# Kernel optimization log

Measured on AMD Instinct MI355X. Metric: run time of the kernel, lower is better.

## Reference

```python
import jax, jax.numpy as jnp
import numpy as np

D_MODEL = 1024
NUM_HEADS = 16
HEAD_DIM = D_MODEL // NUM_HEADS


def setup_inputs() -> dict:
    key = jax.random.key(0)
    ks = jax.random.split(key, 10)
    s = 1.0 / np.sqrt(D_MODEL)
    x = jax.random.normal(ks[0], (2, 2048, D_MODEL), dtype=jnp.float32)
    mask = jax.random.randint(ks[1], (1, 1, 2048, 2048), 0, 2, dtype=jnp.int32)
    Wq = jax.random.uniform(ks[2], (D_MODEL, D_MODEL), jnp.float32, -s, s)
    bq = jnp.zeros((D_MODEL,), jnp.float32)
    Wk = jax.random.uniform(ks[3], (D_MODEL, D_MODEL), jnp.float32, -s, s)
    bk = jnp.zeros((D_MODEL,), jnp.float32)
    Wv = jax.random.uniform(ks[4], (D_MODEL, D_MODEL), jnp.float32, -s, s)
    bv = jnp.zeros((D_MODEL,), jnp.float32)
    Wo = jax.random.uniform(ks[5], (D_MODEL, D_MODEL), jnp.float32, -s, s)
    bo = jnp.zeros((D_MODEL,), jnp.float32)
    return {"x": x, "mask": mask, "Wq": Wq, "bq": bq, "Wk": Wk, "bk": bk,
            "Wv": Wv, "bv": bv, "Wo": Wo, "bo": bo}


def reference(x, mask, Wq, bq, Wk, bk, Wv, bv, Wo, bo):
    B, S, D = x.shape
    # Q/K/V projections, split into heads: [B, H, S, Dh]
    q = (x @ Wq + bq).reshape(B, S, NUM_HEADS, HEAD_DIM).transpose(0, 2, 1, 3)
    k = (x @ Wk + bk).reshape(B, S, NUM_HEADS, HEAD_DIM).transpose(0, 2, 1, 3)
    v = (x @ Wv + bv).reshape(B, S, NUM_HEADS, HEAD_DIM).transpose(0, 2, 1, 3)
    # scores: [B, H, S, S]
    scores = jnp.einsum('bhqd,bhkd->bhqk', q, k) / np.sqrt(HEAD_DIM).astype(np.float32)
    scores = jnp.where(mask == 0, jnp.float32(-1e9), scores)
    weights = jax.nn.softmax(scores, axis=-1)
    # dropout is identity in eval / p=0
    context = jnp.einsum('bhqk,bhkd->bhqd', weights, v)
    context = context.transpose(0, 2, 1, 3).reshape(B, S, D)
    return context @ Wo + bo
```

## Files before the change

kernel.cpp:

```cpp
#include <hip/hip_runtime.h>
#include <stdint.h>

typedef unsigned short u16;
typedef unsigned int u32;
typedef u16 u16x4 __attribute__((ext_vector_type(4)));
typedef u16 u16x8 __attribute__((ext_vector_type(8)));
typedef u32 u32x4 __attribute__((ext_vector_type(4)));
typedef __bf16 bf16x8 __attribute__((ext_vector_type(8)));
typedef float f32x4 __attribute__((ext_vector_type(4)));

#define GLL16(g, l) __builtin_amdgcn_global_load_lds( \
    (const __attribute__((address_space(1))) void*)(g), \
    (__attribute__((address_space(3))) void*)(l), 16, 0, 0)

#define QSCALE 0.18033688011112042f

__device__ __forceinline__ u16 f2bf(float f) {
  u32 u = __builtin_bit_cast(u32, f);
  u += 0x7fffu + ((u >> 16) & 1u);
  return (u16)(u >> 16);
}
__device__ __forceinline__ bf16x8 asbf(u16x8 v) { return __builtin_bit_cast(bf16x8, v); }

__global__ void k_cvt_x(const float* __restrict__ x, u16* __restrict__ o) {
  int i = blockIdx.x * 256 + threadIdx.x;
  f32x4 v = ((const f32x4*)x)[i];
  u16x4 r = { f2bf(v[0]), f2bf(v[1]), f2bf(v[2]), f2bf(v[3]) };
  ((u16x4*)o)[i] = r;
}

__global__ void k_cvt_wT(const float* __restrict__ w, u16* __restrict__ wt, float scale) {
  __shared__ float t[32][33];
  int k0 = blockIdx.x << 5, n0 = blockIdx.y << 5;
  int lx = threadIdx.x & 31, ly = threadIdx.x >> 5;
  #pragma unroll
  for (int i = 0; i < 4; ++i)
    t[ly + 8*i][lx] = w[(size_t)(k0 + ly + 8*i) * 1024 + n0 + lx];
  __syncthreads();
  #pragma unroll
  for (int i = 0; i < 4; ++i)
    wt[(size_t)(n0 + ly + 8*i) * 1024 + k0 + lx] = f2bf(t[lx][ly + 8*i] * scale);
}

__global__ void k_bias(const float* __restrict__ bq, const float* __restrict__ bk,
                       const float* __restrict__ bv, float* __restrict__ o) {
  int i = blockIdx.x * 256 + threadIdx.x;
  float v;
  if (i < 1024) v = bq[i] * QSCALE;
  else if (i < 2048) v = bk[i - 1024];
  else v = bv[i - 2048];
  o[i] = v;
}

__global__ void k_maskbits(const int* __restrict__ mask, u32* __restrict__ bits) {
  int w = blockIdx.x * 256 + threadIdx.x;
  const int* src = mask + (size_t)w * 32;
  u32 b = 0;
  #pragma unroll
  for (int i = 0; i < 32; ++i) b |= (src[i] != 0 ? 1u : 0u) << i;
  bits[w] = b;
}

__global__ __launch_bounds__(256) void k_vT(const u16* __restrict__ vws, u16* __restrict__ vtws) {
  __shared__ u16 t[64][72];
  const int bh = blockIdx.x;
  const int st = blockIdx.y;
  const int tid = threadIdx.x;
  {
    const int s = tid >> 2, c4 = (tid & 3) << 4;
    const u16* src = vws + ((size_t)bh * 2048 + st * 64 + s) * 64 + c4;
    *(u16x8*)&t[s][c4] = *(const u16x8*)src;
    *(u16x8*)&t[s][c4 + 8] = *(const u16x8*)(src + 8);
  }
  __syncthreads();
  {
    const int d = tid >> 2, s0 = (tid & 3) << 4;
    u16 tmp[16];
    #pragma unroll
    for (int j = 0; j < 16; ++j) tmp[j] = t[s0 + j][d];
    u16* dst = vtws + ((size_t)bh * 64 + d) * 2048 + st * 64 + s0;
    *(u16x8*)dst = *(u16x8*)&tmp[0];
    *(u16x8*)(dst + 8) = *(u16x8*)&tmp[8];
  }
}

template<int EPI>
__global__ __launch_bounds__(256)
void k_gemm(const u16* __restrict__ A, const u16* __restrict__ Bt,
            const float* __restrict__ bias, float* __restrict__ outF,
            u16* __restrict__ qws, u16* __restrict__ kws, u16* __restrict__ vws)
{
  __shared__ u16 As[128 * 32];
  __shared__ u16 Bs[128 * 32];
  const int tid = threadIdx.x;
  const int lane = tid & 63;
  const int wv = tid >> 6;
  const int g = lane >> 4, cc = lane & 15;
  const int wr = wv >> 1, wc = wv & 1;
  const int bm = blockIdx.y, bn = blockIdx.x;

  f32x4 acc[4][4] = {};

  for (int k0 = 0; k0 < 1024; k0 += 32) {
    __syncthreads();
    #pragma unroll
    for (int call = 0; call < 2; ++call) {
      int idx = call * 256 + tid;
      int row = idx >> 2;
      int sw = ((idx & 3) << 4) ^ ((row & 3) << 4);
      GLL16((const char*)(A + (size_t)(bm * 128 + row) * 1024 + k0) + sw,
            (char*)As + (call * 256 + wv * 64) * 16);
      GLL16((const char*)(Bt + (size_t)(bn * 128 + row) * 1024 + k0) + sw,
            (char*)Bs + (call * 256 + wv * 64) * 16);
    }
    __syncthreads();

    u16x8 a[4], b[4];
    #pragma unroll
    for (int m = 0; m < 4; ++m) {
      int row = wr * 64 + m * 16 + cc;
      a[m] = *(const u16x8*)((const char*)As + row * 64 + ((g * 16) ^ ((row & 3) << 4)));
    }
    #pragma unroll
    for (int n = 0; n < 4; ++n) {
      int row = wc * 64 + n * 16 + cc;
      b[n] = *(const u16x8*)((const char*)Bs + row * 64 + ((g * 16) ^ ((row & 3) << 4)));
    }
    #pragma unroll
    for (int m = 0; m < 4; ++m)
      #pragma unroll
      for (int n = 0; n < 4; ++n)
        acc[m][n] = __builtin_amdgcn_mfma_f32_16x16x32_bf16(asbf(a[m]), asbf(b[n]), acc[m][n], 0, 0, 0);
  }

  if constexpr (EPI == 1) {
    #pragma unroll
    for (int m = 0; m < 4; ++m) {
      int Mrow0 = bm * 128 + wr * 64 + m * 16 + g * 4;
      #pragma unroll
      for (int n = 0; n < 4; ++n) {
        int Ncol = bn * 128 + wc * 64 + n * 16 + cc;
        float bvv = bias[Ncol];
        #pragma unroll
        for (int r = 0; r < 4; ++r)
          outF[(size_t)(Mrow0 + r) * 1024 + Ncol] = acc[m][n][r] + bvv;
      }
    }
  } else {
    #pragma unroll
    for (int n = 0; n < 4; ++n) {
      int Ncol = bn * 128 + wc * 64 + n * 16 + cc;
      float bvv = bias[Ncol];
      int which = Ncol >> 10;
      int h = (Ncol >> 6) & 15;
      int d = Ncol & 63;
      u16* bp = which == 0 ? qws : (which == 1 ? kws : vws);
      #pragma unroll
      for (int m = 0; m < 4; ++m) {
        int Mrow0 = bm * 128 + wr * 64 + m * 16 + g * 4;
        int bb = Mrow0 >> 11;
        int s0 = Mrow0 & 2047;
        u16* dst = bp + ((size_t)(bb * 16 + h) * 2048 + s0) * 64 + d;
        #pragma unroll
        for (int r = 0; r < 4; ++r) dst[(size_t)r * 64] = f2bf(acc[m][n][r] + bvv);
      }
    }
  }
}

__global__ __launch_bounds__(256, 4)
void k_attn(const u16* __restrict__ qws, const u16* __restrict__ kws,
            const u16* __restrict__ vtws, const u32* __restrict__ mbits,
            u16* __restrict__ ctx)
{
  __shared__ u16 Kt[2][64 * 64];
  __shared__ u16 Vt[2][64 * 64];

  const int tid = threadIdx.x;
  const int lane = tid & 63;
  const int wv = tid >> 6;
  const int g = lane >> 4;
  const int cc = lane & 15;
  const int blk = blockIdx.x;
  const int qc = blk & 31;
  const int bh = blk >> 5;
  const int b = bh >> 4, h = bh & 15;
  const size_t base = (size_t)bh * (2048 * 64);
  const int qrow = qc * 64 + wv * 16;

  u16x8 qf0, qf1;
  {
    const u16* qp = qws + base + (size_t)(qrow + cc) * 64 + g * 8;
    qf0 = *(const u16x8*)qp;
    qf1 = *(const u16x8*)(qp + 32);
  }
  const u32* mq = mbits + (size_t)(qrow + cc) * 64;

  f32x4 oacc[4] = {};
  float lrun = 0.f;

  auto STAGE = [&](int bufi, int kb) {
    #pragma unroll
    for (int call = 0; call < 2; ++call) {
      int idx = call * 256 + tid;
      int row = idx >> 3;
      int sw = ((idx & 7) << 4) ^ ((row & 7) << 4);
      int krow = (row & 32) + (((row >> 2) & 3) << 3) + (((row >> 4) & 1) << 2) + (row & 3);
      GLL16((const char*)(kws + base + (size_t)(kb + krow) * 64) + sw,
            (char*)&Kt[bufi][0] + (call * 256 + wv * 64) * 16);
      GLL16((const char*)(vtws + base + (size_t)row * 2048 + kb) + sw,
            (char*)&Vt[bufi][0] + (call * 256 + wv * 64) * 16);
    }
  };

  STAGE(0, 0);
  __syncthreads();

  int cur = 0;
  for (int kb = 0; kb < 2048; kb += 64) {
    if (kb + 64 < 2048) STAGE(cur ^ 1, kb + 64);

    uint2 mw2 = *(const uint2*)(mq + (kb >> 5));
    u32 m0 = mw2.x >> (g * 8);
    u32 m1 = mw2.y >> (g * 8);

    f32x4 sc[4];
    #pragma unroll
    for (int t = 0; t < 4; ++t) {
      int row = t * 16 + cc;
      int swz = (row & 7) << 4;
      const char* kr = (const char*)&Kt[cur][0] + row * 128;
      u16x8 kf0 = *(const u16x8*)(kr + ((g * 16) ^ swz));
      u16x8 kf1 = *(const u16x8*)(kr + ((g * 16 + 64) ^ swz));
      f32x4 s = {};
      s = __builtin_amdgcn_mfma_f32_16x16x32_bf16(asbf(kf0), asbf(qf0), s, 0, 0, 0);
      s = __builtin_amdgcn_mfma_f32_16x16x32_bf16(asbf(kf1), asbf(qf1), s, 0, 0, 0);
      sc[t] = s;
    }

    float rs = 0.f;
    #pragma unroll
    for (int t = 0; t < 4; ++t) {
      u32 msel = (t >> 1) ? m1 : m0;
      #pragma unroll
      for (int r = 0; r < 4; ++r) {
        float pv = exp2f(sc[t][r]);
        u32 bit = (msel >> (4 * (t & 1) + r)) & 1u;
        pv = bit ? pv : 0.0f;
        sc[t][r] = pv;
        rs += pv;
      }
    }
    u32 pk[8];
    #pragma unroll
    for (int t = 0; t < 4; ++t) {
      u32 w0, w1;
      asm("v_cvt_pk_bf16_f32 %0, %1, %2" : "=v"(w0) : "v"(sc[t][0]), "v"(sc[t][1]));
      asm("v_cvt_pk_bf16_f32 %0, %1, %2" : "=v"(w1) : "v"(sc[t][2]), "v"(sc[t][3]));
      pk[2 * t] = w0;
      pk[2 * t + 1] = w1;
    }
    rs += __shfl_xor(rs, 16);
    rs += __shfl_xor(rs, 32);
    lrun += rs;

    #pragma unroll
    for (int ch = 0; ch < 2; ++ch) {
      u32x4 pw = { pk[4 * ch], pk[4 * ch + 1], pk[4 * ch + 2], pk[4 * ch + 3] };
      u16x8 pa = __builtin_bit_cast(u16x8, pw);
      #pragma unroll
      for (int f = 0; f < 4; ++f) {
        int row = f * 16 + cc;
        int swz = (row & 7) << 4;
        u16x8 vf = *(const u16x8*)((const char*)&Vt[cur][0] + row * 128 + ((g * 16 + ch * 64) ^ swz));
        oacc[f] = __builtin_amdgcn_mfma_f32_16x16x32_bf16(asbf(pa), asbf(vf), oacc[f], 0, 0, 0);
      }
    }

    __syncthreads();
    cur ^= 1;
  }

  float inv = 1.0f / lrun;
  float i_o[4];
  #pragma unroll
  for (int r = 0; r < 4; ++r) i_o[r] = __shfl(inv, 4 * g + r);
  #pragma unroll
  for (int f = 0; f < 4; ++f)
    #pragma unroll
    for (int r = 0; r < 4; ++r) {
      int q = qrow + 4 * g + r;
      ctx[((size_t)(b * 2048 + q)) * 1024 + h * 64 + f * 16 + cc] = f2bf(oacc[f][r] * i_o[r]);
    }
}

extern "C" void kernel_launch(void* const* d_in, const int* in_sizes, int n_in,
                              void* d_out, int out_size, void* d_ws, size_t ws_size,
                              hipStream_t stream) {
  (void)in_sizes; (void)n_in; (void)out_size; (void)ws_size;
  const float* x   = (const float*)d_in[0];
  const int*  mask = (const int*)d_in[1];
  const float* Wq  = (const float*)d_in[2];
  const float* bq  = (const float*)d_in[3];
  const float* Wk  = (const float*)d_in[4];
  const float* bk  = (const float*)d_in[5];
  const float* Wv  = (const float*)d_in[6];
  const float* bv  = (const float*)d_in[7];
  const float* Wo  = (const float*)d_in[8];
  const float* bo  = (const float*)d_in[9];

  char* p = (char*)d_ws;
  size_t off = 0;
  auto carve = [&](size_t n) { char* r = p + off; off = (off + n + 255) & ~(size_t)255; return r; };
  u16*  xb    = (u16*)carve((size_t)4096 * 1024 * 2);
  u16*  wqkvt = (u16*)carve((size_t)3072 * 1024 * 2);
  u16*  wot   = (u16*)carve((size_t)1024 * 1024 * 2);
  float* bqkv = (float*)carve(3072 * 4);
  u32*  mbits = (u32*)carve((size_t)2048 * 64 * 4);
  u16*  qws   = (u16*)carve((size_t)32 * 2048 * 64 * 2);
  u16*  kws   = (u16*)carve((size_t)32 * 2048 * 64 * 2);
  u16*  vws   = (u16*)carve((size_t)32 * 2048 * 64 * 2);
  u16*  vtws  = (u16*)carve((size_t)32 * 2048 * 64 * 2);
  u16*  ctx   = (u16*)carve((size_t)4096 * 1024 * 2);

  k_cvt_x<<<dim3(4096), dim3(256), 0, stream>>>(x, xb);
  k_cvt_wT<<<dim3(32, 32), dim3(256), 0, stream>>>(Wq, wqkvt, QSCALE);
  k_cvt_wT<<<dim3(32, 32), dim3(256), 0, stream>>>(Wk, wqkvt + 1024 * 1024, 1.0f);
  k_cvt_wT<<<dim3(32, 32), dim3(256), 0, stream>>>(Wv, wqkvt + 2 * 1024 * 1024, 1.0f);
  k_cvt_wT<<<dim3(32, 32), dim3(256), 0, stream>>>(Wo, wot, 1.0f);
  k_bias<<<dim3(12), dim3(256), 0, stream>>>(bq, bk, bv, bqkv);
  k_maskbits<<<dim3(512), dim3(256), 0, stream>>>(mask, mbits);

  k_gemm<0><<<dim3(24, 32), dim3(256), 0, stream>>>(xb, wqkvt, bqkv, nullptr, qws, kws, vws);
  k_vT<<<dim3(32, 32), dim3(256), 0, stream>>>(vws, vtws);
  k_attn<<<dim3(1024), dim3(256), 0, stream>>>(qws, kws, vtws, mbits, ctx);
  k_gemm<1><<<dim3(8, 32), dim3(256), 0, stream>>>(ctx, wot, bo, (float*)d_out, nullptr, nullptr, nullptr);
}
```

Measured before the change: 244.3 us.

## Process two 16-row query tiles per wave in attention to reuse K/V LDS loads

Each attention wave now handles 32 query rows (two 16-row tiles) instead of 16, so each block covers 128 queries and the grid halves to 512 blocks. The K and V fragments read from shared memory and the staged K/V tiles are reused across both query tiles, halving LDS reads and global K/V staging per query. The masking select is also replaced with a sign-extended bitfield AND. In exchange, register pressure roughly doubles for accumulators and there are fewer blocks, so fewer waves are available to fill the 256 CUs and hide latency.

```diff
diff --git a/kernel.cpp b/kernel.cpp
--- a/kernel.cpp
+++ b/kernel.cpp
@@ -182,22 +182,26 @@
   const int g = lane >> 4;
   const int cc = lane & 15;
   const int blk = blockIdx.x;
-  const int qc = blk & 31;
-  const int bh = blk >> 5;
+  const int qc = blk & 15;
+  const int bh = blk >> 4;
   const int b = bh >> 4, h = bh & 15;
   const size_t base = (size_t)bh * (2048 * 64);
-  const int qrow = qc * 64 + wv * 16;
-
-  u16x8 qf0, qf1;
+  const int qrow = qc * 128 + wv * 32;
+
+  u16x8 qfA0, qfA1, qfB0, qfB1;
   {
-    const u16* qp = qws + base + (size_t)(qrow + cc) * 64 + g * 8;
-    qf0 = *(const u16x8*)qp;
-    qf1 = *(const u16x8*)(qp + 32);
-  }
-  const u32* mq = mbits + (size_t)(qrow + cc) * 64;
-
-  f32x4 oacc[4] = {};
-  float lrun = 0.f;
+    const u16* qpA = qws + base + (size_t)(qrow + cc) * 64 + g * 8;
+    qfA0 = *(const u16x8*)qpA;
+    qfA1 = *(const u16x8*)(qpA + 32);
+    const u16* qpB = qpA + 16 * 64;
+    qfB0 = *(const u16x8*)qpB;
+    qfB1 = *(const u16x8*)(qpB + 32);
+  }
+  const u32* mqA = mbits + (size_t)(qrow + cc) * 64;
+  const u32* mqB = mqA + 16 * 64;
+
+  f32x4 oaccA[4] = {}, oaccB[4] = {};
+  float lrunA = 0.f, lrunB = 0.f;
 
   auto STAGE = [&](int bufi, int kb) {
     #pragma unroll
@@ -220,11 +224,12 @@
   for (int kb = 0; kb < 2048; kb += 64) {
     if (kb + 64 < 2048) STAGE(cur ^ 1, kb + 64);
 
-    uint2 mw2 = *(const uint2*)(mq + (kb >> 5));
-    u32 m0 = mw2.x >> (g * 8);
-    u32 m1 = mw2.y >> (g * 8);
-
-    f32x4 sc[4];
+    uint2 mwA = *(const uint2*)(mqA + (kb >> 5));
+    uint2 mwB = *(const uint2*)(mqB + (kb >> 5));
+    u32 mA0 = mwA.x >> (g * 8), mA1 = mwA.y >> (g * 8);
+    u32 mB0 = mwB.x >> (g * 8), mB1 = mwB.y >> (g * 8);
+
+    f32x4 scA[4], scB[4];
     #pragma unroll
     for (int t = 0; t < 4; ++t) {
       int row = t * 16 + cc;
@@ -232,48 +237,61 @@
       const char* kr = (const char*)&Kt[cur][0] + row * 128;
       u16x8 kf0 = *(const u16x8*)(kr + ((g * 16) ^ swz));
       u16x8 kf1 = *(const u16x8*)(kr + ((g * 16 + 64) ^ swz));
-      f32x4 s = {};
-      s = __builtin_amdgcn_mfma_f32_16x16x32_bf16(asbf(kf0), asbf(qf0), s, 0, 0, 0);
-      s = __builtin_amdgcn_mfma_f32_16x16x32_bf16(asbf(kf1), asbf(qf1), s, 0, 0, 0);
-      sc[t] = s;
-    }
-
-    float rs = 0.f;
+      f32x4 sA = {}, sB = {};
+      sA = __builtin_amdgcn_mfma_f32_16x16x32_bf16(asbf(kf0), asbf(qfA0), sA, 0, 0, 0);
+      sA = __builtin_amdgcn_mfma_f32_16x16x32_bf16(asbf(kf1), asbf(qfA1), sA, 0, 0, 0);
+      sB = __builtin_amdgcn_mfma_f32_16x16x32_bf16(asbf(kf0), asbf(qfB0), sB, 0, 0, 0);
+      sB = __builtin_amdgcn_mfma_f32_16x16x32_bf16(asbf(kf1), asbf(qfB1), sB, 0, 0, 0);
+      scA[t] = sA;
+      scB[t] = sB;
+    }
+
+    u32 pkA[8], pkB[8];
+    float rsA = 0.f, rsB = 0.f;
     #pragma unroll
     for (int t = 0; t < 4; ++t) {
-      u32 msel = (t >> 1) ? m1 : m0;
+      u32 mselA = (t >> 1) ? mA1 : mA0;
+      u32 mselB = (t >> 1) ? mB1 : mB0;
       #pragma unroll
       for (int r = 0; r < 4; ++r) {
-        float pv = exp2f(sc[t][r]);
-        u32 bit = (msel >> (4 * (t & 1) + r)) & 1u;
-        pv = bit ? pv : 0.0f;
-        sc[t][r] = pv;
-        rs += pv;
+        int sh = 4 * (t & 1) + r;
+        float pA = exp2f(scA[t][r]);
+        float pB = exp2f(scB[t][r]);
+        u32 mmA = (u32)__builtin_amdgcn_sbfe((int)mselA, sh, 1);
+        u32 mmB = (u32)__builtin_amdgcn_sbfe((int)mselB, sh, 1);
+        pA = __builtin_bit_cast(float, __builtin_bit_cast(u32, pA) & mmA);
+        pB = __builtin_bit_cast(float, __builtin_bit_cast(u32, pB) & mmB);
+        scA[t][r] = pA; rsA += pA;
+        scB[t][r] = pB; rsB += pB;
       }
-    }
-    u32 pk[8];
-    #pragma unroll
-    for (int t = 0; t < 4; ++t) {
       u32 w0, w1;
-      asm("v_cvt_pk_bf16_f32 %0, %1, %2" : "=v"(w0) : "v"(sc[t][0]), "v"(sc[t][1]));
-      asm("v_cvt_pk_bf16_f32 %0, %1, %2" : "=v"(w1) : "v"(sc[t][2]), "v"(sc[t][3]));
-      pk[2 * t] = w0;
-      pk[2 * t + 1] = w1;
-    }
-    rs += __shfl_xor(rs, 16);
-    rs += __shfl_xor(rs, 32);
-    lrun += rs;
+      asm("v_cvt_pk_bf16_f32 %0, %1, %2" : "=v"(w0) : "v"(scA[t][0]), "v"(scA[t][1]));
+      asm("v_cvt_pk_bf16_f32 %0, %1, %2" : "=v"(w1) : "v"(scA[t][2]), "v"(scA[t][3]));
+      pkA[2 * t] = w0; pkA[2 * t + 1] = w1;
+      asm("v_cvt_pk_bf16_f32 %0, %1, %2" : "=v"(w0) : "v"(scB[t][0]), "v"(scB[t][1]));
+      asm("v_cvt_pk_bf16_f32 %0, %1, %2" : "=v"(w1) : "v"(scB[t][2]), "v"(scB[t][3]));
+      pkB[2 * t] = w0; pkB[2 * t + 1] = w1;
+    }
+    rsA += __shfl_xor(rsA, 16);
+    rsA += __shfl_xor(rsA, 32);
+    rsB += __shfl_xor(rsB, 16);
+    rsB += __shfl_xor(rsB, 32);
+    lrunA += rsA;
+    lrunB += rsB;
 
     #pragma unroll
     for (int ch = 0; ch < 2; ++ch) {
-      u32x4 pw = { pk[4 * ch], pk[4 * ch + 1], pk[4 * ch + 2], pk[4 * ch + 3] };
-      u16x8 pa = __builtin_bit_cast(u16x8, pw);
+      u32x4 pwA = { pkA[4 * ch], pkA[4 * ch + 1], pkA[4 * ch + 2], pkA[4 * ch + 3] };
+      u32x4 pwB = { pkB[4 * ch], pkB[4 * ch + 1], pkB[4 * ch + 2], pkB[4 * ch + 3] };
+      u16x8 paA = __builtin_bit_cast(u16x8, pwA);
+      u16x8 paB = __builtin_bit_cast(u16x8, pwB);
       #pragma unroll
       for (int f = 0; f < 4; ++f) {
         int row = f * 16 + cc;
         int swz = (row & 7) << 4;
         u16x8 vf = *(const u16x8*)((const char*)&Vt[cur][0] + row * 128 + ((g * 16 + ch * 64) ^ swz));
-        oacc[f] = __builtin_amdgcn_mfma_f32_16x16x32_bf16(asbf(pa), asbf(vf), oacc[f], 0, 0, 0);
+        oaccA[f] = __builtin_amdgcn_mfma_f32_16x16x32_bf16(asbf(paA), asbf(vf), oaccA[f], 0, 0, 0);
+        oaccB[f] = __builtin_amdgcn_mfma_f32_16x16x32_bf16(asbf(paB), asbf(vf), oaccB[f], 0, 0, 0);
       }
     }
 
@@ -281,16 +299,20 @@
     cur ^= 1;
   }
 
-  float inv = 1.0f / lrun;
-  float i_o[4];
-  #pragma unroll
-  for (int r = 0; r < 4; ++r) i_o[r] = __shfl(inv, 4 * g + r);
+  float invA = 1.0f / lrunA, invB = 1.0f / lrunB;
+  float iA[4], iB[4];
+  #pragma unroll
+  for (int r = 0; r < 4; ++r) {
+    iA[r] = __shfl(invA, 4 * g + r);
+    iB[r] = __shfl(invB, 4 * g + r);
+  }
   #pragma unroll
   for (int f = 0; f < 4; ++f)
     #pragma unroll
     for (int r = 0; r < 4; ++r) {
-      int q = qrow + 4 * g + r;
-      ctx[((size_t)(b * 2048 + q)) * 1024 + h * 64 + f * 16 + cc] = f2bf(oacc[f][r] * i_o[r]);
+      int qA = qrow + 4 * g + r;
+      ctx[((size_t)(b * 2048 + qA)) * 1024 + h * 64 + f * 16 + cc] = f2bf(oaccA[f][r] * iA[r]);
+      ctx[((size_t)(b * 2048 + qA + 16)) * 1024 + h * 64 + f * 16 + cc] = f2bf(oaccB[f][r] * iB[r]);
     }
 }
 
@@ -333,6 +355,6 @@
 
   k_gemm<0><<<dim3(24, 32), dim3(256), 0, stream>>>(xb, wqkvt, bqkv, nullptr, qws, kws, vws);
   k_vT<<<dim3(32, 32), dim3(256), 0, stream>>>(vws, vtws);
-  k_attn<<<dim3(1024), dim3(256), 0, stream>>>(qws, kws, vtws, mbits, ctx);
+  k_attn<<<dim3(512), dim3(256), 0, stream>>>(qws, kws, vtws, mbits, ctx);
   k_gemm<1><<<dim3(8, 32), dim3(256), 0, stream>>>(ctx, wot, bo, (float*)d_out, nullptr, nullptr, nullptr);
 }
```

Result: slower. 252.4 us (+3.3%).
